# Performance work log

Hardware: AMD Instinct MI355X
Metric: run time of the kernel (lower is better)

## Reference

```python
import jax, jax.numpy as jnp
import numpy as np

N_NODES = 100000
N_EDGES = 1600000
N_GRAPHS = 64
IN_CH, HID_CH, OUT_CH, N_CLS = 128, 128, 64, 2


def setup_inputs() -> dict:
    key = jax.random.key(0)
    ks = jax.random.split(key, 8)
    x = jax.random.normal(ks[0], (N_NODES, IN_CH), dtype=jnp.float32)
    edge_index = jax.random.randint(ks[1], (2, N_EDGES), 0, N_NODES)
    batch = jnp.sort(jax.random.randint(ks[2], (N_NODES,), 0, N_GRAPHS))
    glorot = lambda k, shp: jax.random.normal(k, shp, dtype=jnp.float32) / np.float32(np.sqrt(shp[0]))
    return {
        "x": x, "edge_index": edge_index, "batch": batch,
        "W1": glorot(ks[3], (IN_CH, HID_CH)), "b1": jnp.zeros((HID_CH,), jnp.float32),
        "W2": glorot(ks[4], (HID_CH, HID_CH)), "b2": jnp.zeros((HID_CH,), jnp.float32),
        "W3": glorot(ks[5], (HID_CH, OUT_CH)), "b3": jnp.zeros((OUT_CH,), jnp.float32),
        "Wfc": glorot(ks[6], (OUT_CH, N_CLS)), "bfc": jnp.zeros((N_CLS,), jnp.float32),
    }


def gcn_conv(x, src, dst, W, b):
    """PyG GCNConv: add self-loops, D^{-1/2} (A+I) D^{-1/2} (x W) + b."""
    n = x.shape[0]
    h = x @ W  # [N, out]
    # degree with self-loops: 1 + in-degree at dst
    deg = jnp.ones((n,), h.dtype).at[dst].add(1.0)
    dinv = jax.lax.rsqrt(deg)  # deg >= 1 always (self-loop)
    norm = dinv[src] * dinv[dst]  # [E]
    agg = jnp.zeros_like(h).at[dst].add(h[src] * norm[:, None])
    agg = agg + h * (dinv * dinv)[:, None]  # self-loop messages
    return agg + b


def global_mean_pool(x, batch, num_graphs):
    s = jax.ops.segment_sum(x, batch, num_segments=num_graphs)
    cnt = jax.ops.segment_sum(jnp.ones((x.shape[0],), x.dtype), batch, num_segments=num_graphs)
    return s / jnp.maximum(cnt, 1.0)[:, None]


def reference(x, edge_index, batch, W1, b1, W2, b2, W3, b3, Wfc, bfc):
    src, dst = edge_index[0], edge_index[1]
    h = jax.nn.relu(gcn_conv(x, src, dst, W1, b1))   # dropout p=0.0 (eval) -> identity
    h = jax.nn.relu(gcn_conv(h, src, dst, W2, b2))
    h = gcn_conv(h, src, dst, W3, b3)
    g = global_mean_pool(h, batch, N_GRAPHS)          # [G, OUT_CH]
    return g @ Wfc + bfc                              # [G, N_CLS]
```

## Files before the change

### kernel.cpp

```cpp
#include <hip/hip_runtime.h>
#include <hip/hip_bf16.h>


#define THREADS 256
#define BSHIFT 9
#define BSIZE 512

typedef __attribute__((ext_vector_type(8))) short short8;
typedef __attribute__((ext_vector_type(16))) float floatx16;

__device__ __forceinline__ unsigned f2bf(float f) {
    unsigned u = __float_as_uint(f);
    return (u + 0x7fffu + ((u >> 16) & 1u)) >> 16;
}

__device__ __forceinline__ void bf8_acc(uint4 v, float* ac) {
    ac[0] += __uint_as_float(v.x << 16);
    ac[1] += __uint_as_float(v.x & 0xffff0000u);
    ac[2] += __uint_as_float(v.y << 16);
    ac[3] += __uint_as_float(v.y & 0xffff0000u);
    ac[4] += __uint_as_float(v.z << 16);
    ac[5] += __uint_as_float(v.z & 0xffff0000u);
    ac[6] += __uint_as_float(v.w << 16);
    ac[7] += __uint_as_float(v.w & 0xffff0000u);
}


__global__ __launch_bounds__(THREADS) void bucket_count(const int* __restrict__ dst,
                                                        int* __restrict__ btotal,
                                                        int E, int nbuck) {
    __shared__ int cnt[BSIZE];
    for (int i = threadIdx.x; i < nbuck; i += THREADS) cnt[i] = 0;
    __syncthreads();
    for (int e = blockIdx.x * THREADS + threadIdx.x; e < E; e += gridDim.x * THREADS)
        atomicAdd(&cnt[dst[e] >> BSHIFT], 1);
    __syncthreads();
    for (int i = threadIdx.x; i < nbuck; i += THREADS) {
        int c = cnt[i];
        if (c) atomicAdd(&btotal[i], c);
    }
}

__global__ __launch_bounds__(512) void bucket_scan(const int* __restrict__ btotal,
                                                   int* __restrict__ bbase,
                                                   int* __restrict__ bcursor,
                                                   float* __restrict__ gsum,
                                                   int nbuck, int E) {
    __shared__ int lds[512];
    int t = threadIdx.x;
    for (int i = t; i < 64 * 64; i += 512) gsum[i] = 0.0f;
    int v = (t < nbuck) ? btotal[t] : 0;
    lds[t] = v;
    __syncthreads();
    for (int off = 1; off < 512; off <<= 1) {
        int tv = (t >= off) ? lds[t - off] : 0;
        __syncthreads();
        lds[t] += tv;
        __syncthreads();
    }
    if (t < nbuck) {
        int excl = lds[t] - v;
        bbase[t] = excl;
        bcursor[t] = excl;
    }
    if (t == 0) bbase[nbuck] = E;
}

__global__ __launch_bounds__(THREADS) void bucket_scatter(const int* __restrict__ src,
                                                          const int* __restrict__ dst,
                                                          int* __restrict__ bcursor,
                                                          int* __restrict__ pairs, int E) {
    __shared__ int cnt[BSIZE];
    __shared__ int base[BSIZE];
    for (int i = threadIdx.x; i < BSIZE; i += THREADS) cnt[i] = 0;
    __syncthreads();
    int e0 = blockIdx.x * 2048;
    int myb[8], myrank[8], mypk[8];
#pragma unroll
    for (int j = 0; j < 8; ++j) {
        int e = e0 + j * THREADS + threadIdx.x;
        myb[j] = -1;
        if (e < E) {
            int d = dst[e];
            mypk[j] = (src[e] << BSHIFT) | (d & (BSIZE - 1));
            myb[j] = d >> BSHIFT;
            myrank[j] = atomicAdd(&cnt[myb[j]], 1);
        }
    }
    __syncthreads();
    for (int i = threadIdx.x; i < BSIZE; i += THREADS) {
        int c = cnt[i];
        base[i] = c ? atomicAdd(&bcursor[i], c) : 0;
    }
    __syncthreads();
#pragma unroll
    for (int j = 0; j < 8; ++j)
        if (myb[j] >= 0) pairs[(size_t)base[myb[j]] + myrank[j]] = mypk[j];
}

__global__ __launch_bounds__(512) void bucket_fill(const int* __restrict__ pairs,
                                                   const int* __restrict__ bbase,
                                                   int* __restrict__ row_start,
                                                   float* __restrict__ dinv,
                                                   int* __restrict__ esrc,
                                                   int N, int E, int nbuck) {
    __shared__ int cnt[BSIZE];
    __shared__ int scn[BSIZE];
    int b = blockIdx.x, t = threadIdx.x;
    int s = bbase[b], e = bbase[b + 1];
    cnt[t] = 0;
    __syncthreads();
    for (int i = s + t; i < e; i += 512) atomicAdd(&cnt[pairs[i] & (BSIZE - 1)], 1);
    __syncthreads();
    int v = cnt[t];
    scn[t] = v;
    __syncthreads();
    for (int off = 1; off < 512; off <<= 1) {
        int tv = (t >= off) ? scn[t - off] : 0;
        __syncthreads();
        scn[t] += tv;
        __syncthreads();
    }
    int excl = scn[t] - v;
    int g = (b << BSHIFT) + t;
    if (g < N) {
        row_start[g] = s + excl;
        dinv[g] = rsqrtf(1.0f + (float)v);
    }
    if (b == nbuck - 1 && t == 0) row_start[N] = E;
    scn[t] = excl;
    __syncthreads();
    for (int i = s + t; i < e; i += 512) {
        int p = pairs[i];
        int r = atomicAdd(&scn[p & (BSIZE - 1)], 1);
        esrc[s + r] = ((unsigned)p) >> BSHIFT;
    }
}

__device__ __forceinline__ void wt_pack(const float* W, uint4* Wtp, int C, int li) {
    int c = li >> 4, ch = li & 15;
    unsigned r[8];
#pragma unroll
    for (int j = 0; j < 8; ++j) r[j] = f2bf(W[(size_t)(ch * 8 + j) * C + c]);
    uint4 o;
    o.x = r[0] | (r[1] << 16);
    o.y = r[2] | (r[3] << 16);
    o.z = r[4] | (r[5] << 16);
    o.w = r[6] | (r[7] << 16);
    Wtp[li] = o;
}

__global__ __launch_bounds__(THREADS) void prep_wt_all(const float* __restrict__ W1,
                                                       const float* __restrict__ W2,
                                                       const float* __restrict__ W3,
                                                       uint4* __restrict__ Wt1,
                                                       uint4* __restrict__ Wt2,
                                                       uint4* __restrict__ Wt3) {
    int idx = blockIdx.x * THREADS + threadIdx.x;
    if (idx < 2048) wt_pack(W1, Wt1, 128, idx);
    else if (idx < 4096) wt_pack(W2, Wt2, 128, idx - 2048);
    else if (idx < 5120) wt_pack(W3, Wt3, 64, idx - 4096);
}

__global__ __launch_bounds__(THREADS) void prep_x(const float* __restrict__ x,
                                                  const float* __restrict__ dinv,
                                                  uint4* __restrict__ Z, int n) {
    int idx = blockIdx.x * THREADS + threadIdx.x;
    if (idx >= n * 16) return;
    int r = idx >> 4, c = idx & 15;
    float dv = dinv[r];
    const float* p = x + (size_t)r * 128 + c * 8;
    float4 a = *(const float4*)p;
    float4 b = *(const float4*)(p + 4);
    uint4 o;
    o.x = f2bf(a.x * dv) | (f2bf(a.y * dv) << 16);
    o.y = f2bf(a.z * dv) | (f2bf(a.w * dv) << 16);
    o.z = f2bf(b.x * dv) | (f2bf(b.y * dv) << 16);
    o.w = f2bf(b.z * dv) | (f2bf(b.w * dv) << 16);
    Z[idx] = o;
}

__global__ __launch_bounds__(THREADS) void fused_layer(const uint4* __restrict__ Z,
                                                       const uint4* __restrict__ Wt,
                                                       const int* __restrict__ row_start,
                                                       const int* __restrict__ esrc,
                                                       const float* __restrict__ dinv,
                                                       const float* __restrict__ bias,
                                                       uint4* __restrict__ out, int n) {
    __shared__ __align__(16) uint4 ldsX[64 * 16];
    int row0 = blockIdx.x * 64;
    int maxr = n - row0;
    if (maxr > 64) maxr = 64;
    int tid = threadIdx.x;
    int lane = tid & 15, grp = tid >> 4;

    for (int round = 0; round < 4; ++round) {
        int r = round * 16 + grp;
        int node = row0 + r;
        int nd = (node < n) ? node : (n - 1);
        float ac[8] = {0, 0, 0, 0, 0, 0, 0, 0};
        bf8_acc(Z[(size_t)nd * 16 + lane], ac);
        int s = row_start[nd], e = row_start[nd + 1];
        int i = s;
        for (; i + 8 <= e; i += 8) {
            int s0 = esrc[i], s1 = esrc[i + 1], s2 = esrc[i + 2], s3 = esrc[i + 3];
            int s4 = esrc[i + 4], s5 = esrc[i + 5], s6 = esrc[i + 6], s7 = esrc[i + 7];
            uint4 v0 = Z[(size_t)s0 * 16 + lane];
            uint4 v1 = Z[(size_t)s1 * 16 + lane];
            uint4 v2 = Z[(size_t)s2 * 16 + lane];
            uint4 v3 = Z[(size_t)s3 * 16 + lane];
            uint4 v4 = Z[(size_t)s4 * 16 + lane];
            uint4 v5 = Z[(size_t)s5 * 16 + lane];
            uint4 v6 = Z[(size_t)s6 * 16 + lane];
            uint4 v7 = Z[(size_t)s7 * 16 + lane];
            bf8_acc(v0, ac); bf8_acc(v1, ac); bf8_acc(v2, ac); bf8_acc(v3, ac);
            bf8_acc(v4, ac); bf8_acc(v5, ac); bf8_acc(v6, ac); bf8_acc(v7, ac);
        }
        for (; i + 4 <= e; i += 4) {
            int s0 = esrc[i], s1 = esrc[i + 1], s2 = esrc[i + 2], s3 = esrc[i + 3];
            uint4 v0 = Z[(size_t)s0 * 16 + lane];
            uint4 v1 = Z[(size_t)s1 * 16 + lane];
            uint4 v2 = Z[(size_t)s2 * 16 + lane];
            uint4 v3 = Z[(size_t)s3 * 16 + lane];
            bf8_acc(v0, ac); bf8_acc(v1, ac); bf8_acc(v2, ac); bf8_acc(v3, ac);
        }
        for (; i < e; ++i) bf8_acc(Z[(size_t)esrc[i] * 16 + lane], ac);
        float dv = dinv[nd];
        uint4 o;
        o.x = f2bf(ac[0] * dv) | (f2bf(ac[1] * dv) << 16);
        o.y = f2bf(ac[2] * dv) | (f2bf(ac[3] * dv) << 16);
        o.z = f2bf(ac[4] * dv) | (f2bf(ac[5] * dv) << 16);
        o.w = f2bf(ac[6] * dv) | (f2bf(ac[7] * dv) << 16);
        ldsX[r * 16 + (lane ^ (r & 7))] = o;
    }
    __syncthreads();

    int l = tid & 63, wv = tid >> 6;
    int l31 = l & 31, half = l >> 5;
    int nt = wv & 1, mt0 = (wv >> 1) * 2;
    floatx16 acc[2];
#pragma unroll
    for (int t = 0; t < 2; ++t)
#pragma unroll
        for (int q = 0; q < 16; ++q) acc[t][q] = 0.0f;
    int xrow = nt * 32 + l31, xsw = xrow & 7;
#pragma unroll
    for (int kt = 0; kt < 8; ++kt) {
        int chunk = kt * 2 + half;
        short8 xf = *(const short8*)&ldsX[xrow * 16 + (chunk ^ xsw)];
#pragma unroll
        for (int t = 0; t < 2; ++t) {
            int c = (mt0 + t) * 32 + l31;
            short8 wf = *(const short8*)&Wt[c * 16 + chunk];
            acc[t] = __builtin_amdgcn_mfma_f32_32x32x16_bf16(wf, xf, acc[t], 0, 0, 0);
        }
    }
    __syncthreads();

    int node = nt * 32 + l31;
    float dv = (node < maxr) ? dinv[row0 + node] : 0.0f;
    char* outb = (char*)ldsX;
#pragma unroll
    for (int t = 0; t < 2; ++t) {
        int cb = (mt0 + t) * 32;
#pragma unroll
        for (int q = 0; q < 4; ++q) {
            float v[4];
#pragma unroll
            for (int m = 0; m < 4; ++m) {
                int ch = cb + 8 * q + 4 * half + m;
                float x_ = acc[t][q * 4 + m] + bias[ch];
                x_ = fmaxf(x_, 0.0f);
                v[m] = x_ * dv;
            }
            uint2 pk = make_uint2(f2bf(v[0]) | (f2bf(v[1]) << 16),
                                  f2bf(v[2]) | (f2bf(v[3]) << 16));
            int chunk = (cb >> 3) + q;
            *(uint2*)(outb + node * 256 + ((chunk ^ (node & 7)) * 16) + half * 8) = pk;
        }
    }
    __syncthreads();
    for (int idx = tid; idx < maxr * 16; idx += THREADS) {
        int r = idx >> 4, c = idx & 15;
        out[(size_t)(row0 + r) * 16 + c] = *(uint4*)(outb + r * 256 + ((c ^ (r & 7)) * 16));
    }
}

__global__ __launch_bounds__(THREADS) void gemm3(const uint4* __restrict__ Z,
                                                 const uint4* __restrict__ Wt,
                                                 uint4* __restrict__ out, int n) {
    __shared__ __align__(16) uint4 ldsX[64 * 16];
    int row0 = blockIdx.x * 64;
    int maxr = n - row0;
    if (maxr > 64) maxr = 64;
    int tid = threadIdx.x;
    for (int idx = tid; idx < 1024; idx += THREADS) {
        int r = idx >> 4, c = idx & 15;
        uint4 o = (r < maxr) ? Z[(size_t)(row0 + r) * 16 + c] : make_uint4(0, 0, 0, 0);
        ldsX[r * 16 + (c ^ (r & 7))] = o;
    }
    __syncthreads();
    int l = tid & 63, wv = tid >> 6;
    int l31 = l & 31, half = l >> 5;
    int nt = wv & 1, mt = wv >> 1;
    floatx16 acc;
#pragma unroll
    for (int q = 0; q < 16; ++q) acc[q] = 0.0f;
    int xrow = nt * 32 + l31, xsw = xrow & 7;
#pragma unroll
    for (int kt = 0; kt < 8; ++kt) {
        int chunk = kt * 2 + half;
        short8 xf = *(const short8*)&ldsX[xrow * 16 + (chunk ^ xsw)];
        int c = mt * 32 + l31;
        short8 wf = *(const short8*)&Wt[c * 16 + chunk];
        acc = __builtin_amdgcn_mfma_f32_32x32x16_bf16(wf, xf, acc, 0, 0, 0);
    }
    __syncthreads();
    int node = nt * 32 + l31;
    char* outb = (char*)ldsX;
    int cb = mt * 32;
#pragma unroll
    for (int q = 0; q < 4; ++q) {
        uint2 pk = make_uint2(f2bf(acc[q * 4 + 0]) | (f2bf(acc[q * 4 + 1]) << 16),
                              f2bf(acc[q * 4 + 2]) | (f2bf(acc[q * 4 + 3]) << 16));
        int chunk = (cb >> 3) + q;
        *(uint2*)(outb + node * 128 + ((chunk ^ (node & 7)) * 16) + half * 8) = pk;
    }
    __syncthreads();
    for (int idx = tid; idx < maxr * 8; idx += THREADS) {
        int r = idx >> 3, c = idx & 7;
        out[(size_t)(row0 + r) * 8 + c] = *(uint4*)(outb + r * 128 + ((c ^ (r & 7)) * 16));
    }
}

__global__ __launch_bounds__(THREADS) void agg_pool(const uint4* __restrict__ Ps,
                                                    const int* __restrict__ row_start,
                                                    const int* __restrict__ esrc,
                                                    const float* __restrict__ dinv,
                                                    const float* __restrict__ bias,
                                                    const int* __restrict__ batch,
                                                    float* __restrict__ gsum, int n) {
    __shared__ float gpart[32][65];
    __shared__ int used[32];
    int tid = threadIdx.x;
    int lane = tid & 7, grp = tid >> 3;
    int node = blockIdx.x * 32 + grp;
    if (tid < 32) used[tid] = 0;
    for (int idx = tid; idx < 2048; idx += THREADS) gpart[idx >> 6][idx & 63] = 0.0f;
    __syncthreads();
    int gmin = batch[blockIdx.x * 32];
    if (node < n) {
        float ac[8] = {0, 0, 0, 0, 0, 0, 0, 0};
        bf8_acc(Ps[(size_t)node * 8 + lane], ac);
        int s = row_start[node], e = row_start[node + 1];
        int i = s;
        for (; i + 8 <= e; i += 8) {
            int s0 = esrc[i], s1 = esrc[i + 1], s2 = esrc[i + 2], s3 = esrc[i + 3];
            int s4 = esrc[i + 4], s5 = esrc[i + 5], s6 = esrc[i + 6], s7 = esrc[i + 7];
            uint4 v0 = Ps[(size_t)s0 * 8 + lane];
            uint4 v1 = Ps[(size_t)s1 * 8 + lane];
            uint4 v2 = Ps[(size_t)s2 * 8 + lane];
            uint4 v3 = Ps[(size_t)s3 * 8 + lane];
            uint4 v4 = Ps[(size_t)s4 * 8 + lane];
            uint4 v5 = Ps[(size_t)s5 * 8 + lane];
            uint4 v6 = Ps[(size_t)s6 * 8 + lane];
            uint4 v7 = Ps[(size_t)s7 * 8 + lane];
            bf8_acc(v0, ac); bf8_acc(v1, ac); bf8_acc(v2, ac); bf8_acc(v3, ac);
            bf8_acc(v4, ac); bf8_acc(v5, ac); bf8_acc(v6, ac); bf8_acc(v7, ac);
        }
        for (; i + 4 <= e; i += 4) {
            int s0 = esrc[i], s1 = esrc[i + 1], s2 = esrc[i + 2], s3 = esrc[i + 3];
            uint4 v0 = Ps[(size_t)s0 * 8 + lane];
            uint4 v1 = Ps[(size_t)s1 * 8 + lane];
            uint4 v2 = Ps[(size_t)s2 * 8 + lane];
            uint4 v3 = Ps[(size_t)s3 * 8 + lane];
            bf8_acc(v0, ac); bf8_acc(v1, ac); bf8_acc(v2, ac); bf8_acc(v3, ac);
        }
        for (; i < e; ++i) bf8_acc(Ps[(size_t)esrc[i] * 8 + lane], ac);
        float dv = dinv[node];
        float4 b0 = ((const float4*)bias)[lane * 2];
        float4 b1 = ((const float4*)bias)[lane * 2 + 1];
        float h[8];
        h[0] = fmaf(dv, ac[0], b0.x); h[1] = fmaf(dv, ac[1], b0.y);
        h[2] = fmaf(dv, ac[2], b0.z); h[3] = fmaf(dv, ac[3], b0.w);
        h[4] = fmaf(dv, ac[4], b1.x); h[5] = fmaf(dv, ac[5], b1.y);
        h[6] = fmaf(dv, ac[6], b1.z); h[7] = fmaf(dv, ac[7], b1.w);
        int g = batch[node];
        int slot = g - gmin;
        if (slot < 32) {
            if (lane == 0) used[slot] = 1;
#pragma unroll
            for (int j = 0; j < 8; ++j) atomicAdd(&gpart[slot][lane * 8 + j], h[j]);
        } else {
#pragma unroll
            for (int j = 0; j < 8; ++j) atomicAdd(&gsum[(size_t)g * 64 + lane * 8 + j], h[j]);
        }
    }
    __syncthreads();
    for (int idx = tid; idx < 2048; idx += THREADS) {
        int s = idx >> 6, ch = idx & 63;
        if (used[s]) atomicAdd(&gsum[(size_t)(gmin + s) * 64 + ch], gpart[s][ch]);
    }
}

__device__ __forceinline__ int dev_lower_bound(const int* a, int n, int key) {
    int lo = 0, hi = n;
    while (lo < hi) {
        int mid = (lo + hi) >> 1;
        if (a[mid] < key) lo = mid + 1;
        else hi = mid;
    }
    return lo;
}

__global__ __launch_bounds__(128) void finalize_fc(const float* __restrict__ gsum,
                                                   const int* __restrict__ batch, int n,
                                                   const float* __restrict__ Wfc,
                                                   const float* __restrict__ bfc,
                                                   float* __restrict__ out) {
    __shared__ float gm[64 * 64];
    __shared__ float cnt[64];
    int t = threadIdx.x;
    if (t < 64)
        cnt[t] = (float)(dev_lower_bound(batch, n, t + 1) - dev_lower_bound(batch, n, t));
    __syncthreads();
    for (int i = t; i < 64 * 64; i += 128) gm[i] = gsum[i] / fmaxf(cnt[i >> 6], 1.0f);
    __syncthreads();
    int g = t >> 1, cls = t & 1;
    float acc = bfc[cls];
    for (int c = 0; c < 64; ++c) acc = fmaf(gm[g * 64 + c], Wfc[c * 2 + cls], acc);
    out[g * 2 + cls] = acc;
}

extern "C" void kernel_launch(void* const* d_in, const int* in_sizes, int n_in,
                              void* d_out, int out_size, void* d_ws, size_t ws_size,
                              hipStream_t stream) {
    const float* x    = (const float*)d_in[0];
    const int*   ei   = (const int*)d_in[1];
    const int*   batch= (const int*)d_in[2];
    const float* W1   = (const float*)d_in[3];
    const float* b1   = (const float*)d_in[4];
    const float* W2   = (const float*)d_in[5];
    const float* b2   = (const float*)d_in[6];
    const float* W3   = (const float*)d_in[7];
    const float* b3   = (const float*)d_in[8];
    const float* Wfc  = (const float*)d_in[9];
    const float* bfc  = (const float*)d_in[10];
    float* out = (float*)d_out;

    const int N = in_sizes[2];
    const int E = in_sizes[1] / 2;
    const int* esrc_in = ei;
    const int* edst_in = ei + E;
    const int nbuck = (N + BSIZE - 1) >> BSHIFT;

    uint4* bufA      = (uint4*)d_ws;
    uint4* bufB      = bufA + (size_t)N * 16;
    uint4* bufC      = bufB + (size_t)N * 16;
    int*   pairs     = (int*)(bufC + (size_t)N * 8);
    int*   esrc      = pairs + E;
    int*   row_start = esrc + E;
    float* dinv      = (float*)(row_start + N + 1);
    int*   btotal    = (int*)(dinv + N);
    int*   bbase     = btotal + 512;
    int*   bcursor   = bbase + 513;
    float* gsum      = (float*)(bcursor + 512);
    uint4* Wt1       = (uint4*)(gsum + 64 * 64);
    uint4* Wt2       = Wt1 + 2048;
    uint4* Wt3       = Wt2 + 2048;

    hipMemsetAsync(btotal, 0, 512 * sizeof(int), stream);
    bucket_count<<<512, THREADS, 0, stream>>>(edst_in, btotal, E, nbuck);
    bucket_scan<<<1, 512, 0, stream>>>(btotal, bbase, bcursor, gsum, nbuck, E);
    bucket_scatter<<<(E + 2047) / 2048, THREADS, 0, stream>>>(esrc_in, edst_in, bcursor, pairs, E);
    bucket_fill<<<nbuck, 512, 0, stream>>>(pairs, bbase, row_start, dinv, esrc, N, E, nbuck);
    prep_wt_all<<<20, THREADS, 0, stream>>>(W1, W2, W3, Wt1, Wt2, Wt3);
    prep_x<<<(N * 16 + THREADS - 1) / THREADS, THREADS, 0, stream>>>(x, dinv, bufA, N);

    const int GB = (N + 63) / 64;

    fused_layer<<<GB, THREADS, 0, stream>>>(bufA, Wt1, row_start, esrc, dinv, b1, bufB, N);
    fused_layer<<<GB, THREADS, 0, stream>>>(bufB, Wt2, row_start, esrc, dinv, b2, bufA, N);
    gemm3<<<GB, THREADS, 0, stream>>>(bufA, Wt3, bufC, N);
    agg_pool<<<(N + 31) / 32, THREADS, 0, stream>>>(bufC, row_start, esrc, dinv, b3, batch, gsum, N);

    finalize_fc<<<1, 128, 0, stream>>>(gsum, batch, N, Wfc, bfc, out);
}
```

Baseline: 429.6 us.

## Software-pipeline gather across rows with double-buffered edge and feature loads

Replaces the per-row gather loop in the fused layer with a flattened, double-buffered pipeline. Each thread group streams edge indices and neighbour feature rows for its four nodes in fixed chunks of eight, issuing the next chunk's loads before accumulating the current one, and redirects out-of-range slots to a zeroed dummy row. The aim is to hide gather latency and remove the tail loops and row-boundary stalls. In exchange it raises register pressure and wastes loads on padded slots.

```diff
diff --git a/kernel.cpp b/kernel.cpp
--- a/kernel.cpp
+++ b/kernel.cpp
@@ -45,10 +45,12 @@
                                                    int* __restrict__ bbase,
                                                    int* __restrict__ bcursor,
                                                    float* __restrict__ gsum,
+                                                   float* __restrict__ zrow,
                                                    int nbuck, int E) {
     __shared__ int lds[512];
     int t = threadIdx.x;
     for (int i = t; i < 64 * 64; i += 512) gsum[i] = 0.0f;
+    if (t < 64) zrow[t] = 0.0f;
     int v = (t < nbuck) ? btotal[t] : 0;
     lds[t] = v;
     __syncthreads();
@@ -180,12 +182,62 @@
     Z[idx] = o;
 }
 
+
+#define GCN_ISSUE_E(EB, CB, CE, FIN)                                    \
+    {                                                                   \
+        CB = cI; CE = Ecur;                                             \
+        _Pragma("unroll") for (int j_ = 0; j_ < 8; ++j_) {              \
+            int idx_ = CB + j_;                                         \
+            EB[j_] = esrc[idx_ < CE ? idx_ : 0];                        \
+        }                                                               \
+        cI += 8;                                                        \
+        FIN = (cI >= Ecur);                                             \
+        if (FIN) {                                                      \
+            ++rI; cI = Sx1; Ecur = Ex1;                                 \
+            Sx1 = Sx2; Ex1 = Ex2; Sx2 = Sx3; Ex2 = Ex3;                 \
+        }                                                               \
+    }
+
+#define GCN_ISSUE_Z(ZB, EB, CB, CE)                                    \
+    {                                                                   \
+        _Pragma("unroll") for (int j_ = 0; j_ < 8; ++j_) {              \
+            const uint4* p_ = (CB + j_ < CE)                            \
+                                  ? (Z + ((size_t)EB[j_] * 16 + lane))  \
+                                  : zl;                                 \
+            ZB[j_] = *p_;                                               \
+        }                                                               \
+    }
+
+#define GCN_CONSUME(ZB, FINZ)                                           \
+    {                                                                   \
+        bf8_acc(ZB[0], ac); bf8_acc(ZB[1], ac);                         \
+        bf8_acc(ZB[2], ac); bf8_acc(ZB[3], ac);                         \
+        bf8_acc(ZB[4], ac); bf8_acc(ZB[5], ac);                         \
+        bf8_acc(ZB[6], ac); bf8_acc(ZB[7], ac);                         \
+        if (FINZ) {                                                     \
+            float dv_ = dv0;                                            \
+            uint4 o_;                                                   \
+            o_.x = f2bf(ac[0] * dv_) | (f2bf(ac[1] * dv_) << 16);       \
+            o_.y = f2bf(ac[2] * dv_) | (f2bf(ac[3] * dv_) << 16);       \
+            o_.z = f2bf(ac[4] * dv_) | (f2bf(ac[5] * dv_) << 16);       \
+            o_.w = f2bf(ac[6] * dv_) | (f2bf(ac[7] * dv_) << 16);       \
+            int tr_ = rcon * 16 + grp;                                  \
+            ldsX[tr_ * 16 + (lane ^ (tr_ & 7))] = o_;                   \
+            ++rcon;                                                     \
+            dv0 = dv1; dv1 = dv2; dv2 = dv3;                            \
+            _Pragma("unroll") for (int q_ = 0; q_ < 8; ++q_) ac[q_] = 0.0f; \
+            bf8_acc(self1, ac);                                         \
+            self1 = self2; self2 = self3;                               \
+        }                                                               \
+    }
+
 __global__ __launch_bounds__(THREADS) void fused_layer(const uint4* __restrict__ Z,
                                                        const uint4* __restrict__ Wt,
                                                        const int* __restrict__ row_start,
                                                        const int* __restrict__ esrc,
                                                        const float* __restrict__ dinv,
                                                        const float* __restrict__ bias,
+                                                       const uint4* __restrict__ zrow,
                                                        uint4* __restrict__ out, int n) {
     __shared__ __align__(16) uint4 ldsX[64 * 16];
     int row0 = blockIdx.x * 64;
@@ -194,44 +246,44 @@
     int tid = threadIdx.x;
     int lane = tid & 15, grp = tid >> 4;
 
-    for (int round = 0; round < 4; ++round) {
-        int r = round * 16 + grp;
-        int node = row0 + r;
-        int nd = (node < n) ? node : (n - 1);
-        float ac[8] = {0, 0, 0, 0, 0, 0, 0, 0};
-        bf8_acc(Z[(size_t)nd * 16 + lane], ac);
-        int s = row_start[nd], e = row_start[nd + 1];
-        int i = s;
-        for (; i + 8 <= e; i += 8) {
-            int s0 = esrc[i], s1 = esrc[i + 1], s2 = esrc[i + 2], s3 = esrc[i + 3];
-            int s4 = esrc[i + 4], s5 = esrc[i + 5], s6 = esrc[i + 6], s7 = esrc[i + 7];
-            uint4 v0 = Z[(size_t)s0 * 16 + lane];
-            uint4 v1 = Z[(size_t)s1 * 16 + lane];
-            uint4 v2 = Z[(size_t)s2 * 16 + lane];
-            uint4 v3 = Z[(size_t)s3 * 16 + lane];
-            uint4 v4 = Z[(size_t)s4 * 16 + lane];
-            uint4 v5 = Z[(size_t)s5 * 16 + lane];
-            uint4 v6 = Z[(size_t)s6 * 16 + lane];
-            uint4 v7 = Z[(size_t)s7 * 16 + lane];
-            bf8_acc(v0, ac); bf8_acc(v1, ac); bf8_acc(v2, ac); bf8_acc(v3, ac);
-            bf8_acc(v4, ac); bf8_acc(v5, ac); bf8_acc(v6, ac); bf8_acc(v7, ac);
-        }
-        for (; i + 4 <= e; i += 4) {
-            int s0 = esrc[i], s1 = esrc[i + 1], s2 = esrc[i + 2], s3 = esrc[i + 3];
-            uint4 v0 = Z[(size_t)s0 * 16 + lane];
-            uint4 v1 = Z[(size_t)s1 * 16 + lane];
-            uint4 v2 = Z[(size_t)s2 * 16 + lane];
-            uint4 v3 = Z[(size_t)s3 * 16 + lane];
-            bf8_acc(v0, ac); bf8_acc(v1, ac); bf8_acc(v2, ac); bf8_acc(v3, ac);
-        }
-        for (; i < e; ++i) bf8_acc(Z[(size_t)esrc[i] * 16 + lane], ac);
-        float dv = dinv[nd];
-        uint4 o;
-        o.x = f2bf(ac[0] * dv) | (f2bf(ac[1] * dv) << 16);
-        o.y = f2bf(ac[2] * dv) | (f2bf(ac[3] * dv) << 16);
-        o.z = f2bf(ac[4] * dv) | (f2bf(ac[5] * dv) << 16);
-        o.w = f2bf(ac[6] * dv) | (f2bf(ac[7] * dv) << 16);
-        ldsX[r * 16 + (lane ^ (r & 7))] = o;
+    int nm1 = n - 1;
+    int nd0 = row0 + grp;       if (nd0 > nm1) nd0 = nm1;
+    int nd1 = row0 + grp + 16;  if (nd1 > nm1) nd1 = nm1;
+    int nd2 = row0 + grp + 32;  if (nd2 > nm1) nd2 = nm1;
+    int nd3 = row0 + grp + 48;  if (nd3 > nm1) nd3 = nm1;
+
+    uint4 self0 = Z[(size_t)nd0 * 16 + lane];
+    uint4 self1 = Z[(size_t)nd1 * 16 + lane];
+    uint4 self2 = Z[(size_t)nd2 * 16 + lane];
+    uint4 self3 = Z[(size_t)nd3 * 16 + lane];
+    float dv0 = dinv[nd0], dv1 = dinv[nd1], dv2 = dinv[nd2], dv3 = dinv[nd3];
+    int cI = row_start[nd0], Ecur = row_start[nd0 + 1];
+    int Sx1 = row_start[nd1], Ex1 = row_start[nd1 + 1];
+    int Sx2 = row_start[nd2], Ex2 = row_start[nd2 + 1];
+    int Sx3 = row_start[nd3], Ex3 = row_start[nd3 + 1];
+
+    const uint4* zl = zrow + lane;
+    int rI = 0, rcon = 0;
+    float ac[8] = {0, 0, 0, 0, 0, 0, 0, 0};
+    bf8_acc(self0, ac);
+
+    int eb0[8], eb1[8];
+    uint4 Zb0[8], Zb1[8];
+    int b0 = 0, x0 = 0, b1 = 0, x1 = 0;
+    bool f0e = false, f1e = false, fz0 = false, fz1 = false;
+    bool e0 = false, e1 = false, z0h = false, z1h = false;
+
+    if (rI < 4) { GCN_ISSUE_E(eb0, b0, x0, f0e); e0 = true; }
+    if (rI < 4) { GCN_ISSUE_E(eb1, b1, x1, f1e); e1 = true; }
+    if (e0) { GCN_ISSUE_Z(Zb0, eb0, b0, x0); fz0 = f0e; z0h = true; e0 = false; }
+
+    while (__any(rcon < 4)) {
+        if (rI < 4) { GCN_ISSUE_E(eb0, b0, x0, f0e); e0 = true; }
+        if (e1) { GCN_ISSUE_Z(Zb1, eb1, b1, x1); fz1 = f1e; z1h = true; e1 = false; }
+        if (z0h) { GCN_CONSUME(Zb0, fz0); z0h = false; }
+        if (rI < 4) { GCN_ISSUE_E(eb1, b1, x1, f1e); e1 = true; }
+        if (e0) { GCN_ISSUE_Z(Zb0, eb0, b0, x0); fz0 = f0e; z0h = true; e0 = false; }
+        if (z1h) { GCN_CONSUME(Zb1, fz1); z1h = false; }
     }
     __syncthreads();
 
@@ -285,6 +337,10 @@
         out[(size_t)(row0 + r) * 16 + c] = *(uint4*)(outb + r * 256 + ((c ^ (r & 7)) * 16));
     }
 }
+
+#undef GCN_ISSUE_E
+#undef GCN_ISSUE_Z
+#undef GCN_CONSUME
 
 __global__ __launch_bounds__(THREADS) void gemm3(const uint4* __restrict__ Z,
                                                  const uint4* __restrict__ Wt,
@@ -468,10 +524,11 @@
     uint4* Wt1       = (uint4*)(gsum + 64 * 64);
     uint4* Wt2       = Wt1 + 2048;
     uint4* Wt3       = Wt2 + 2048;
+    float* zrow      = (float*)(Wt3 + 1024);
 
     hipMemsetAsync(btotal, 0, 512 * sizeof(int), stream);
     bucket_count<<<512, THREADS, 0, stream>>>(edst_in, btotal, E, nbuck);
-    bucket_scan<<<1, 512, 0, stream>>>(btotal, bbase, bcursor, gsum, nbuck, E);
+    bucket_scan<<<1, 512, 0, stream>>>(btotal, bbase, bcursor, gsum, zrow, nbuck, E);
     bucket_scatter<<<(E + 2047) / 2048, THREADS, 0, stream>>>(esrc_in, edst_in, bcursor, pairs, E);
     bucket_fill<<<nbuck, 512, 0, stream>>>(pairs, bbase, row_start, dinv, esrc, N, E, nbuck);
     prep_wt_all<<<20, THREADS, 0, stream>>>(W1, W2, W3, Wt1, Wt2, Wt3);
@@ -479,8 +536,10 @@
 
     const int GB = (N + 63) / 64;
 
-    fused_layer<<<GB, THREADS, 0, stream>>>(bufA, Wt1, row_start, esrc, dinv, b1, bufB, N);
-    fused_layer<<<GB, THREADS, 0, stream>>>(bufB, Wt2, row_start, esrc, dinv, b2, bufA, N);
+    fused_layer<<<GB, THREADS, 0, stream>>>(bufA, Wt1, row_start, esrc, dinv, b1,
+                                            (const uint4*)zrow, bufB, N);
+    fused_layer<<<GB, THREADS, 0, stream>>>(bufB, Wt2, row_start, esrc, dinv, b2,
+                                            (const uint4*)zrow, bufA, N);
     gemm3<<<GB, THREADS, 0, stream>>>(bufA, Wt3, bufC, N);
     agg_pool<<<(N + 31) / 32, THREADS, 0, stream>>>(bufC, row_start, esrc, dinv, b3, batch, gsum, N);
 
```

Measured after the change: 446.7 us. +4.0%, slower.
